# Performance work log

Measured on AMD Instinct MI355X. Metric: run time of the kernel, lower is better.

## Reference

```python
import jax, jax.numpy as jnp
import numpy as np

ALPHA = 0.3  # LeakyReLU slope


def setup_inputs() -> dict:
    key = jax.random.key(0)
    k1, k2, k3, k4 = jax.random.split(key, 4)
    B, S, F, H = 256, 8, 2048, 8
    inputs = jax.random.normal(k1, (B, S, F), dtype=jnp.float32)
    # GlorotNormal-ish scale for W: std = sqrt(2/(2F+F))
    W = jax.random.normal(k2, (H, 2 * F, F), dtype=jnp.float32) * np.float32(np.sqrt(2.0 / (3 * F)))
    att_w = jax.random.normal(k3, (H, F), dtype=jnp.float32) * np.float32(np.sqrt(2.0 / (F + 1)))
    bias = jax.random.normal(k4, (H, F), dtype=jnp.float32) * 0.01
    return {"inputs": inputs, "W": W, "att_w": att_w, "bias": bias}


def reference(inputs, W, att_w, bias):
    # inputs: [B,S,F]; W: [H,2F,F]; att_w: [H,F]; bias: [H,F]
    B, S, F = inputs.shape
    # h_chunk = node 0 features repeated along seq axis, concat with h -> [B,S,2F]
    h_chunk = jnp.broadcast_to(inputs[:, :1, :], (B, S, F))
    h_cat = jnp.concatenate([h_chunk, inputs], axis=-1)
    # per-head projection + LeakyReLU (GATv2 ordering): [B,H,S,F]
    Wh = jax.nn.leaky_relu(jnp.einsum('bsc,hcf->bhsf', h_cat, W), negative_slope=ALPHA)
    # attention scores e: [B,H,S]; softmax over seq axis (axis=1 in original layout)
    e = jnp.einsum('bhsf,hf->bhs', Wh, att_w)
    attn = jax.nn.softmax(e, axis=-1)
    # broadcast-multiply, bias add, residual, identity activation
    att_out = attn[..., None] * Wh + bias[None, :, None, :] + inputs[:, None, :, :]
    # sum over heads / num_heads == mean over heads
    return att_out.mean(axis=1)
```

## Files before the change

kernel.cpp:

```cpp
#include <hip/hip_runtime.h>
#include <stdint.h>


typedef __attribute__((ext_vector_type(4))) float f32x4;
typedef __attribute__((ext_vector_type(8))) short bf16x8;
typedef __attribute__((ext_vector_type(4))) unsigned short u16x4;
typedef unsigned short u16;
typedef unsigned int u32;

#define LRELU_ALPHA 0.3f

__device__ __forceinline__ u16 bf16_rn(float x) {
  u32 u = __float_as_uint(x);
  u32 r = 0x7FFFu + ((u >> 16) & 1u);
  return (u16)((u + r) >> 16);
}
__device__ __forceinline__ float bf16_to_f32(u16 h) {
  return __uint_as_float(((u32)h) << 16);
}

__global__ __launch_bounds__(256) void split_x_kernel(
    const float* __restrict__ X, u16* __restrict__ Xhi, u16* __restrict__ Xlo) {
  int idx = (blockIdx.x * 256 + threadIdx.x) * 4;
  f32x4 v = *(const f32x4*)&X[idx];
  u16x4 hi, lo;
#pragma unroll
  for (int j = 0; j < 4; ++j) {
    u16 h = bf16_rn(v[j]);
    hi[j] = h;
    lo[j] = bf16_rn(v[j] - bf16_to_f32(h));
  }
  *(u16x4*)&Xhi[idx] = hi;
  *(u16x4*)&Xlo[idx] = lo;
}

__global__ __launch_bounds__(256) void transpose_split_w(
    const float* __restrict__ W, u16* __restrict__ Whi, u16* __restrict__ Wlo) {
  __shared__ float tile[64][65];
  int bid = blockIdx.x;
  int h = bid >> 11;
  int t = bid & 2047;
  int ct = t & 63;
  int ft = t >> 6;
  int c0 = ct << 6, f0 = ft << 6;
  int tid = threadIdx.x;
  int rr = tid >> 4;
  int q4 = (tid & 15) << 2;
  const float* src = W + (size_t)(h * 4096 + c0) * 2048 + f0;
#pragma unroll
  for (int it = 0; it < 4; ++it) {
    int r = it * 16 + rr;
    f32x4 v = *(const f32x4*)&src[(size_t)r * 2048 + q4];
    tile[r][q4] = v[0]; tile[r][q4 + 1] = v[1];
    tile[r][q4 + 2] = v[2]; tile[r][q4 + 3] = v[3];
  }
  __syncthreads();
  size_t dst = (size_t)(h * 2048 + f0) * 4096 + c0;
#pragma unroll
  for (int it = 0; it < 4; ++it) {
    int fr = it * 16 + rr;
    u16x4 hi, lo;
#pragma unroll
    for (int j = 0; j < 4; ++j) {
      float a = tile[q4 + j][fr];
      u16 hb = bf16_rn(a);
      hi[j] = hb;
      lo[j] = bf16_rn(a - bf16_to_f32(hb));
    }
    *(u16x4*)&Whi[dst + (size_t)fr * 4096 + q4] = hi;
    *(u16x4*)&Wlo[dst + (size_t)fr * 4096 + q4] = lo;
  }
}

__device__ __forceinline__ void gl_lds16(const u16* g, u16* l) {
  __builtin_amdgcn_global_load_lds(
      (const __attribute__((address_space(1))) void*)g,
      (__attribute__((address_space(3))) void*)l, 16, 0, 0);
}

template <int AST, bool EPI2>
__global__ __launch_bounds__(256) void gemm_split3(
    const u16* __restrict__ Ahi, const u16* __restrict__ Alo,
    const u16* __restrict__ Bhi, const u16* __restrict__ Blo,
    const float* __restrict__ proj0, float* __restrict__ C,
    int Mdim, int koff) {
  __shared__ alignas(16) u16 lAhi[128 * 32];
  __shared__ alignas(16) u16 lAlo[128 * 32];
  __shared__ alignas(16) u16 lBhi[128 * 32];
  __shared__ alignas(16) u16 lBlo[128 * 32];

  int tid = threadIdx.x;
  int lane = tid & 63;
  int w = tid >> 6;

  int nwg = gridDim.x;
  int bid = blockIdx.x;
  int wg = (bid & 7) * (nwg >> 3) + (bid >> 3);
  int MT = Mdim >> 7;
  int nt = wg / MT;
  int mt = wg - nt * MT;
  int m0 = mt << 7, n0 = nt << 7;

  int srow = lane >> 2;
  int sunit = lane & 3;
  int r0 = w * 32 + srow;
  int r1 = r0 + 16;
  size_t qc0 = (size_t)((sunit ^ (r0 & 3)) << 3);
  size_t qc1 = (size_t)((sunit ^ (r1 & 3)) << 3);
  size_t offA0 = (size_t)(m0 + r0) * AST + qc0;
  size_t offA1 = (size_t)(m0 + r1) * AST + qc1;
  size_t offB0 = (size_t)(n0 + r0) * 4096 + (size_t)koff + qc0;
  size_t offB1 = (size_t)(n0 + r1) * 4096 + (size_t)koff + qc1;
  const int lds0 = w * 1024;
  const int lds1 = lds0 + 512;

  f32x4 acc[4][4];
#pragma unroll
  for (int i = 0; i < 4; ++i)
#pragma unroll
    for (int j = 0; j < 4; ++j) acc[i][j] = (f32x4){0.f, 0.f, 0.f, 0.f};

  const int wr = w >> 1, wc = w & 1;
  const int frow = lane & 15;
  const int kgrp = lane >> 4;

  int aidx[4], bidx[4];
#pragma unroll
  for (int i = 0; i < 4; ++i) {
    int ar = wr * 64 + i * 16 + frow;
    aidx[i] = ar * 32 + ((kgrp ^ (ar & 3)) << 3);
    int br = wc * 64 + i * 16 + frow;
    bidx[i] = br * 32 + ((kgrp ^ (br & 3)) << 3);
  }

  for (int kt = 0; kt < 64; ++kt) {
    size_t ko = (size_t)kt * 32;
    gl_lds16(Ahi + offA0 + ko, &lAhi[lds0]);
    gl_lds16(Ahi + offA1 + ko, &lAhi[lds1]);
    gl_lds16(Alo + offA0 + ko, &lAlo[lds0]);
    gl_lds16(Alo + offA1 + ko, &lAlo[lds1]);
    gl_lds16(Bhi + offB0 + ko, &lBhi[lds0]);
    gl_lds16(Bhi + offB1 + ko, &lBhi[lds1]);
    gl_lds16(Blo + offB0 + ko, &lBlo[lds0]);
    gl_lds16(Blo + offB1 + ko, &lBlo[lds1]);
    __syncthreads();

    bf16x8 ah[4], al[4], bh[4], bl[4];
#pragma unroll
    for (int i = 0; i < 4; ++i) {
      ah[i] = *(const bf16x8*)&lAhi[aidx[i]];
      al[i] = *(const bf16x8*)&lAlo[aidx[i]];
      bh[i] = *(const bf16x8*)&lBhi[bidx[i]];
      bl[i] = *(const bf16x8*)&lBlo[bidx[i]];
    }
#pragma unroll
    for (int i = 0; i < 4; ++i)
#pragma unroll
      for (int j = 0; j < 4; ++j) {
        acc[i][j] = __builtin_amdgcn_mfma_f32_16x16x32_bf16(ah[i], bh[j], acc[i][j], 0, 0, 0);
        acc[i][j] = __builtin_amdgcn_mfma_f32_16x16x32_bf16(ah[i], bl[j], acc[i][j], 0, 0, 0);
        acc[i][j] = __builtin_amdgcn_mfma_f32_16x16x32_bf16(al[i], bh[j], acc[i][j], 0, 0, 0);
      }
    __syncthreads();
  }

#pragma unroll
  for (int i = 0; i < 4; ++i) {
    int gmb = m0 + wr * 64 + i * 16 + kgrp * 4;
#pragma unroll
    for (int j = 0; j < 4; ++j) {
      int gn = n0 + wc * 64 + j * 16 + frow;
#pragma unroll
      for (int r = 0; r < 4; ++r) {
        float v = acc[i][j][r];
        int gm = gmb + r;
        if constexpr (EPI2) {
          v += proj0[(size_t)(gm >> 3) * 16384 + gn];
          v = v > 0.f ? v : v * LRELU_ALPHA;
        }
        C[(size_t)gm * 16384 + gn] = v;
      }
    }
  }
}

__global__ __launch_bounds__(256) void esoftmax_kernel(
    const float* __restrict__ Wh, const float* __restrict__ att_w,
    float* __restrict__ attn) {
  int bid = blockIdx.x;
  int b = bid >> 3, h = bid & 7;
  int tid = threadIdx.x, lane = tid & 63, w = tid >> 6;
  __shared__ float ev[8];
  const float* aw = att_w + h * 2048;
#pragma unroll
  for (int si = 0; si < 2; ++si) {
    int s = w * 2 + si;
    const float* row = Wh + (size_t)((b * 8 + s) * 8 + h) * 2048;
    float sum = 0.f;
#pragma unroll
    for (int i = 0; i < 8; ++i) {
      int idx = (i * 64 + lane) * 4;
      f32x4 rv = *(const f32x4*)&row[idx];
      f32x4 av = *(const f32x4*)&aw[idx];
      sum += rv[0] * av[0] + rv[1] * av[1] + rv[2] * av[2] + rv[3] * av[3];
    }
#pragma unroll
    for (int off = 32; off > 0; off >>= 1) sum += __shfl_down(sum, off, 64);
    if (lane == 0) ev[s] = sum;
  }
  __syncthreads();
  if (tid == 0) {
    float mx = ev[0];
#pragma unroll
    for (int s = 1; s < 8; ++s) mx = fmaxf(mx, ev[s]);
    float ex[8], den = 0.f;
#pragma unroll
    for (int s = 0; s < 8; ++s) { ex[s] = expf(ev[s] - mx); den += ex[s]; }
    float inv = 1.f / den;
#pragma unroll
    for (int s = 0; s < 8; ++s) attn[b * 64 + h * 8 + s] = ex[s] * inv;
  }
}

__global__ __launch_bounds__(256) void out_kernel(
    const float* __restrict__ X, const float* __restrict__ bias,
    const float* __restrict__ Wh, const float* __restrict__ attn,
    float* __restrict__ out) {
  int bid = blockIdx.x;
  int m = bid >> 1;
  int half = bid & 1;
  int b = m >> 3, s = m & 7;
  int f0 = half * 1024 + threadIdx.x * 4;
  __shared__ float a_sm[8];
  if (threadIdx.x < 8) a_sm[threadIdx.x] = attn[b * 64 + threadIdx.x * 8 + s];
  __syncthreads();
  f32x4 acc = *(const f32x4*)&X[(size_t)m * 2048 + f0];
  f32x4 hs = {0.f, 0.f, 0.f, 0.f};
#pragma unroll
  for (int h = 0; h < 8; ++h) {
    f32x4 wv = *(const f32x4*)&Wh[(size_t)m * 16384 + h * 2048 + f0];
    f32x4 bv = *(const f32x4*)&bias[h * 2048 + f0];
    hs += wv * a_sm[h] + bv;
  }
  acc += hs * 0.125f;
  *(f32x4*)&out[(size_t)m * 2048 + f0] = acc;
}

extern "C" void kernel_launch(void* const* d_in, const int* in_sizes, int n_in,
                              void* d_out, int out_size, void* d_ws, size_t ws_size,
                              hipStream_t stream) {
  const float* X = (const float*)d_in[0];
  const float* W = (const float*)d_in[1];
  const float* att_w = (const float*)d_in[2];
  const float* bias = (const float*)d_in[3];
  float* out = (float*)d_out;

  char* ws = (char*)d_ws;
  u16* Whi = (u16*)ws;
  u16* Wlo = (u16*)(ws + 134217728ull);
  u16* Xhi = (u16*)(ws + 268435456ull);
  u16* Xlo = (u16*)(ws + 276824064ull);
  float* proj0 = (float*)(ws + 285212672ull);
  float* Wh = (float*)(ws + 301989888ull);
  float* attn = (float*)(ws + 436207616ull);

  split_x_kernel<<<4096, 256, 0, stream>>>(X, Xhi, Xlo);
  transpose_split_w<<<16384, 256, 0, stream>>>(W, Whi, Wlo);
  gemm_split3<16384, false><<<256, 256, 0, stream>>>(Xhi, Xlo, Whi, Wlo, nullptr, proj0, 256, 0);
  gemm_split3<2048, true><<<2048, 256, 0, stream>>>(Xhi, Xlo, Whi, Wlo, proj0, Wh, 2048, 2048);
  esoftmax_kernel<<<2048, 256, 0, stream>>>(Wh, att_w, attn);
  out_kernel<<<4096, 256, 0, stream>>>(X, bias, Wh, attn, out);
}
```

Measured before the change: 986.5 us.

## Rewrite split-bf16 GEMM with 256x256 tiles, double-buffered LDS and interleaved staging

Replaces the 128x128 single-buffered split-bf16 GEMM with a 256x256-tile, 512-thread kernel that double-buffers LDS and stages hi and lo operands separately. Global-to-LDS loads for the next k-step are issued between the three MFMA passes, with explicit vmcnt waits, raw barriers and setprio around the MFMA bursts. The larger tile halves global traffic per FLOP and hides load latency behind compute. In exchange it uses 128 KB of LDS and many more accumulator registers, and the small first GEMM now runs only 64 workgroups, which may underfill the GPU.

```diff
diff --git a/kernel.cpp b/kernel.cpp
--- a/kernel.cpp
+++ b/kernel.cpp
@@ -78,102 +78,158 @@
       (__attribute__((address_space(3))) void*)l, 16, 0, 0);
 }
 
+#define BAR()    asm volatile("s_barrier" ::: "memory")
+#define VM4BAR() asm volatile("s_waitcnt vmcnt(4)\n\ts_barrier" ::: "memory")
+#define VM0BAR() asm volatile("s_waitcnt vmcnt(0)\n\ts_barrier" ::: "memory")
+
 template <int AST, bool EPI2>
-__global__ __launch_bounds__(256) void gemm_split3(
+__global__ __launch_bounds__(512, 2) void gemm3p(
     const u16* __restrict__ Ahi, const u16* __restrict__ Alo,
     const u16* __restrict__ Bhi, const u16* __restrict__ Blo,
     const float* __restrict__ proj0, float* __restrict__ C,
     int Mdim, int koff) {
-  __shared__ alignas(16) u16 lAhi[128 * 32];
-  __shared__ alignas(16) u16 lAlo[128 * 32];
-  __shared__ alignas(16) u16 lBhi[128 * 32];
-  __shared__ alignas(16) u16 lBlo[128 * 32];
-
-  int tid = threadIdx.x;
-  int lane = tid & 63;
-  int w = tid >> 6;
-
-  int nwg = gridDim.x;
-  int bid = blockIdx.x;
-  int wg = (bid & 7) * (nwg >> 3) + (bid >> 3);
-  int MT = Mdim >> 7;
-  int nt = wg / MT;
-  int mt = wg - nt * MT;
-  int m0 = mt << 7, n0 = nt << 7;
-
-  int srow = lane >> 2;
-  int sunit = lane & 3;
-  int r0 = w * 32 + srow;
-  int r1 = r0 + 16;
-  size_t qc0 = (size_t)((sunit ^ (r0 & 3)) << 3);
-  size_t qc1 = (size_t)((sunit ^ (r1 & 3)) << 3);
-  size_t offA0 = (size_t)(m0 + r0) * AST + qc0;
-  size_t offA1 = (size_t)(m0 + r1) * AST + qc1;
-  size_t offB0 = (size_t)(n0 + r0) * 4096 + (size_t)koff + qc0;
-  size_t offB1 = (size_t)(n0 + r1) * 4096 + (size_t)koff + qc1;
-  const int lds0 = w * 1024;
-  const int lds1 = lds0 + 512;
-
-  f32x4 acc[4][4];
-#pragma unroll
-  for (int i = 0; i < 4; ++i)
+  __shared__ alignas(16) u16 lAh[2][8192];
+  __shared__ alignas(16) u16 lAl[2][8192];
+  __shared__ alignas(16) u16 lBh[2][8192];
+  __shared__ alignas(16) u16 lBl[2][8192];
+
+  const int tid = threadIdx.x;
+  const int lane = tid & 63;
+  const int w = tid >> 6;
+
+  const int nwg = gridDim.x;
+  const int bid = blockIdx.x;
+  const int wg = (bid & 7) * (nwg >> 3) + (bid >> 3);
+  const int MT = Mdim >> 8;
+  const int nt = wg / MT;
+  const int mt = wg - nt * MT;
+  const int m0 = mt << 8, n0 = nt << 8;
+
+  const int c0i = 2 * w, c1i = 2 * w + 1;
+  const int r0 = c0i * 16 + (lane >> 2);
+  const int r1 = c1i * 16 + (lane >> 2);
+  const int ul0 = ((lane & 3) - (r0 >> 1)) & 3;
+  const int ul1 = ((lane & 3) - (r1 >> 1)) & 3;
+  const size_t sA0 = (size_t)(m0 + r0) * AST + ul0 * 8;
+  const size_t sA1 = (size_t)(m0 + r1) * AST + ul1 * 8;
+  const size_t sB0 = (size_t)(n0 + r0) * 4096 + (size_t)koff + ul0 * 8;
+  const size_t sB1 = (size_t)(n0 + r1) * 4096 + (size_t)koff + ul1 * 8;
+  const int cw0 = c0i * 512, cw1 = c1i * 512;
+
+  auto stageHi = [&](int b, size_t ko) {
+    gl_lds16(Ahi + sA0 + ko, &lAh[b][cw0]);
+    gl_lds16(Ahi + sA1 + ko, &lAh[b][cw1]);
+    gl_lds16(Bhi + sB0 + ko, &lBh[b][cw0]);
+    gl_lds16(Bhi + sB1 + ko, &lBh[b][cw1]);
+  };
+  auto stageLo = [&](int b, size_t ko) {
+    gl_lds16(Alo + sA0 + ko, &lAl[b][cw0]);
+    gl_lds16(Alo + sA1 + ko, &lAl[b][cw1]);
+    gl_lds16(Blo + sB0 + ko, &lBl[b][cw0]);
+    gl_lds16(Blo + sB1 + ko, &lBl[b][cw1]);
+  };
+
+  const int frow = lane & 15, kgrp = lane >> 4;
+  const int wr = w >> 2, wc = w & 3;
+  int aoff[8], boff[4];
+#pragma unroll
+  for (int i = 0; i < 8; ++i) {
+    int r = wr * 128 + i * 16 + frow;
+    aoff[i] = r * 32 + ((kgrp + (r >> 1)) & 3) * 8;
+  }
+#pragma unroll
+  for (int j = 0; j < 4; ++j) {
+    int r = wc * 64 + j * 16 + frow;
+    boff[j] = r * 32 + ((kgrp + (r >> 1)) & 3) * 8;
+  }
+
+  f32x4 acc[8][4];
+#pragma unroll
+  for (int i = 0; i < 8; ++i)
 #pragma unroll
     for (int j = 0; j < 4; ++j) acc[i][j] = (f32x4){0.f, 0.f, 0.f, 0.f};
 
-  const int wr = w >> 1, wc = w & 1;
-  const int frow = lane & 15;
-  const int kgrp = lane >> 4;
-
-  int aidx[4], bidx[4];
-#pragma unroll
-  for (int i = 0; i < 4; ++i) {
-    int ar = wr * 64 + i * 16 + frow;
-    aidx[i] = ar * 32 + ((kgrp ^ (ar & 3)) << 3);
-    int br = wc * 64 + i * 16 + frow;
-    bidx[i] = br * 32 + ((kgrp ^ (br & 3)) << 3);
-  }
-
-  for (int kt = 0; kt < 64; ++kt) {
-    size_t ko = (size_t)kt * 32;
-    gl_lds16(Ahi + offA0 + ko, &lAhi[lds0]);
-    gl_lds16(Ahi + offA1 + ko, &lAhi[lds1]);
-    gl_lds16(Alo + offA0 + ko, &lAlo[lds0]);
-    gl_lds16(Alo + offA1 + ko, &lAlo[lds1]);
-    gl_lds16(Bhi + offB0 + ko, &lBhi[lds0]);
-    gl_lds16(Bhi + offB1 + ko, &lBhi[lds1]);
-    gl_lds16(Blo + offB0 + ko, &lBlo[lds0]);
-    gl_lds16(Blo + offB1 + ko, &lBlo[lds1]);
-    __syncthreads();
-
-    bf16x8 ah[4], al[4], bh[4], bl[4];
-#pragma unroll
-    for (int i = 0; i < 4; ++i) {
-      ah[i] = *(const bf16x8*)&lAhi[aidx[i]];
-      al[i] = *(const bf16x8*)&lAlo[aidx[i]];
-      bh[i] = *(const bf16x8*)&lBhi[bidx[i]];
-      bl[i] = *(const bf16x8*)&lBlo[bidx[i]];
-    }
-#pragma unroll
-    for (int i = 0; i < 4; ++i)
+  stageHi(0, 0);
+  stageLo(0, 0);
+  VM4BAR();
+
+  bf16x8 ah[8], al[8], bh[4], bl[4];
+
+  for (int kt = 0; kt < 63; ++kt) {
+    const int p = kt & 1, q = p ^ 1;
+    const size_t ko = (size_t)(kt + 1) * 32;
+#pragma unroll
+    for (int i = 0; i < 8; ++i) ah[i] = *(const bf16x8*)&lAh[p][aoff[i]];
+#pragma unroll
+    for (int j = 0; j < 4; ++j) bh[j] = *(const bf16x8*)&lBh[p][boff[j]];
+    stageHi(q, ko);
+    BAR();
+    __builtin_amdgcn_s_setprio(1);
+#pragma unroll
+    for (int i = 0; i < 8; ++i)
+#pragma unroll
+      for (int j = 0; j < 4; ++j)
+        acc[i][j] = __builtin_amdgcn_mfma_f32_16x16x32_bf16(ah[i], bh[j], acc[i][j], 0, 0, 0);
+    __builtin_amdgcn_s_setprio(0);
+    VM4BAR();
+
+#pragma unroll
+    for (int j = 0; j < 4; ++j) bl[j] = *(const bf16x8*)&lBl[p][boff[j]];
+    stageLo(q, ko);
+    BAR();
+    __builtin_amdgcn_s_setprio(1);
+#pragma unroll
+    for (int i = 0; i < 8; ++i)
+#pragma unroll
+      for (int j = 0; j < 4; ++j)
+        acc[i][j] = __builtin_amdgcn_mfma_f32_16x16x32_bf16(ah[i], bl[j], acc[i][j], 0, 0, 0);
+    __builtin_amdgcn_s_setprio(0);
+    BAR();
+
+#pragma unroll
+    for (int i = 0; i < 8; ++i) al[i] = *(const bf16x8*)&lAl[p][aoff[i]];
+    BAR();
+    __builtin_amdgcn_s_setprio(1);
+#pragma unroll
+    for (int i = 0; i < 8; ++i)
+#pragma unroll
+      for (int j = 0; j < 4; ++j)
+        acc[i][j] = __builtin_amdgcn_mfma_f32_16x16x32_bf16(al[i], bh[j], acc[i][j], 0, 0, 0);
+    __builtin_amdgcn_s_setprio(0);
+    VM4BAR();
+  }
+
+  VM0BAR();
+  {
+    const int p = 1;
+#pragma unroll
+    for (int i = 0; i < 8; ++i) ah[i] = *(const bf16x8*)&lAh[p][aoff[i]];
+#pragma unroll
+    for (int j = 0; j < 4; ++j) bh[j] = *(const bf16x8*)&lBh[p][boff[j]];
+#pragma unroll
+    for (int j = 0; j < 4; ++j) bl[j] = *(const bf16x8*)&lBl[p][boff[j]];
+#pragma unroll
+    for (int i = 0; i < 8; ++i) al[i] = *(const bf16x8*)&lAl[p][aoff[i]];
+#pragma unroll
+    for (int i = 0; i < 8; ++i)
 #pragma unroll
       for (int j = 0; j < 4; ++j) {
         acc[i][j] = __builtin_amdgcn_mfma_f32_16x16x32_bf16(ah[i], bh[j], acc[i][j], 0, 0, 0);
         acc[i][j] = __builtin_amdgcn_mfma_f32_16x16x32_bf16(ah[i], bl[j], acc[i][j], 0, 0, 0);
         acc[i][j] = __builtin_amdgcn_mfma_f32_16x16x32_bf16(al[i], bh[j], acc[i][j], 0, 0, 0);
       }
-    __syncthreads();
-  }
-
-#pragma unroll
-  for (int i = 0; i < 4; ++i) {
-    int gmb = m0 + wr * 64 + i * 16 + kgrp * 4;
+  }
+
+#pragma unroll
+  for (int i = 0; i < 8; ++i) {
+    const int gmb = m0 + wr * 128 + i * 16 + kgrp * 4;
 #pragma unroll
     for (int j = 0; j < 4; ++j) {
-      int gn = n0 + wc * 64 + j * 16 + frow;
+      const int gn = n0 + wc * 64 + j * 16 + frow;
 #pragma unroll
       for (int r = 0; r < 4; ++r) {
         float v = acc[i][j][r];
-        int gm = gmb + r;
+        const int gm = gmb + r;
         if constexpr (EPI2) {
           v += proj0[(size_t)(gm >> 3) * 16384 + gn];
           v = v > 0.f ? v : v * LRELU_ALPHA;
@@ -266,8 +322,8 @@
 
   split_x_kernel<<<4096, 256, 0, stream>>>(X, Xhi, Xlo);
   transpose_split_w<<<16384, 256, 0, stream>>>(W, Whi, Wlo);
-  gemm_split3<16384, false><<<256, 256, 0, stream>>>(Xhi, Xlo, Whi, Wlo, nullptr, proj0, 256, 0);
-  gemm_split3<2048, true><<<2048, 256, 0, stream>>>(Xhi, Xlo, Whi, Wlo, proj0, Wh, 2048, 2048);
+  gemm3p<16384, false><<<64, 512, 0, stream>>>(Xhi, Xlo, Whi, Wlo, nullptr, proj0, 256, 0);
+  gemm3p<2048, true><<<512, 512, 0, stream>>>(Xhi, Xlo, Whi, Wlo, proj0, Wh, 2048, 2048);
   esoftmax_kernel<<<2048, 256, 0, stream>>>(Wh, att_w, attn);
   out_kernel<<<4096, 256, 0, stream>>>(X, bias, Wh, attn, out);
 }
```

Result: faster. 966.1 us (-2.1%).
